# Kernel tuning notes

Measured on AMD Instinct MI355X. Metric: run time of the kernel, lower is better.

Reference implementation:

```python
import jax, jax.numpy as jnp
import numpy as np

N = 32768  # number of leaf states (rows); power of 2 for a clean Fenwick tree
D = 256    # embed_dim


def tree_cell(W, b, hl, cl, hr, cr):
    """Binary TreeLSTM cell: gates from [h_l; h_r], per-child forget gates."""
    z = jnp.concatenate([hl, hr], axis=-1) @ W + b  # [*, 5D]
    i, o, u, fl, fr = jnp.split(z, 5, axis=-1)
    c = jax.nn.sigmoid(i) * jnp.tanh(u) + jax.nn.sigmoid(fl) * cl + jax.nn.sigmoid(fr) * cr
    h = jax.nn.sigmoid(o) * jnp.tanh(c)
    return h, c


def setup_inputs() -> dict:
    key = jax.random.key(0)
    ks = jax.random.split(key, 6)
    s = 0.05  # glorot-ish scale for 512-fan-in weights
    return {
        "h_bot": jax.random.normal(ks[0], (N, D), jnp.float32),
        "c_bot": jax.random.normal(ks[1], (N, D), jnp.float32),
        "W_merge": jax.random.normal(ks[2], (2 * D, 5 * D), jnp.float32) * s,
        "b_merge": jnp.zeros((5 * D,), jnp.float32),
        "W_sum": jax.random.normal(ks[3], (2 * D, 5 * D), jnp.float32) * s,
        "b_sum": jnp.zeros((5 * D,), jnp.float32),
    }


def _fenwick(h_bot, c_bot, W_merge, b_merge, W_sum, b_sum):
    L = N.bit_length() - 1  # 15 tree levels above the leaves
    # --- build Fenwick tree: level k node j covers leaves [j*2^k, (j+1)*2^k) ---
    levels_h, levels_c = [h_bot], [c_bot]
    for k in range(1, L + 1):
        ph, pc = levels_h[-1], levels_c[-1]
        h, c = tree_cell(W_merge, b_merge, ph[0::2], pc[0::2], ph[1::2], pc[1::2])
        levels_h.append(h)
        levels_c.append(c)
    # --- per-prefix summary: for each t in 1..N fold the set-bit nodes of t ---
    # (matches FenwickTree.forward: levels ascending, state = summary(state, node))
    t = jnp.arange(1, N + 1)
    state_h = jnp.zeros((N, D), h_bot.dtype)
    state_c = jnp.zeros((N, D), h_bot.dtype)
    valid = jnp.zeros((N,), bool)
    for k in range(L + 1):
        has = (((t >> k) & 1) == 1)
        # node covering the trailing 2^k block of prefix t at level k
        idx = jnp.clip((t >> (k + 1)) * 2, 0, levels_h[k].shape[0] - 1)
        node_h = levels_h[k][idx]  # irregular gather  [N, D]
        node_c = levels_c[k][idx]
        nh, nc = tree_cell(W_sum, b_sum, state_h, state_c, node_h, node_c)
        m, v = has[:, None], valid[:, None]
        state_h = jnp.where(m, jnp.where(v, nh, node_h), state_h)
        state_c = jnp.where(m, jnp.where(v, nc, node_c), state_c)
        valid = valid | has
    return jnp.concatenate([state_h, state_c], axis=-1)  # [N, 2D]: (row_h, row_c)


def reference(h_bot, c_bot, W_merge, b_merge, W_sum, b_sum):
    return _fenwick(h_bot, c_bot, W_merge, b_merge, W_sum, b_sum)
```

## Files before the change

kernel.cpp:

```cpp
#include <hip/hip_runtime.h>
#include <hip/hip_bf16.h>


typedef unsigned short u16;
typedef unsigned int u32;
using short8  = __attribute__((ext_vector_type(8))) short;
using float4v = __attribute__((ext_vector_type(4))) float;


__device__ __forceinline__ u16 f2bf(float f) {
  u32 u = __float_as_uint(f);
  u = (u + 0x7FFFu + ((u >> 16) & 1u)) >> 16;
  return (u16)u;
}
__device__ __forceinline__ float bf2f(u16 h) {
  return __uint_as_float(((u32)h) << 16);
}
__device__ __forceinline__ float sigf(float x) { return 1.0f / (1.0f + __expf(-x)); }
__device__ __forceinline__ float tanhfast(float x) {
  return 2.0f / (1.0f + __expf(-2.0f * x)) - 1.0f;
}

__device__ __forceinline__ void async16(const void* g, void* l) {
  __builtin_amdgcn_global_load_lds((const __attribute__((address_space(1))) void*)g,
                                   (__attribute__((address_space(3))) void*)l,
                                   16, 0, 0);
}

__device__ __forceinline__ void row_srcs(int mode, int k, int row,
                                         const u16* h0b, const u16* hlv,
                                         const u16* sthA, const u16* sthB,
                                         const u16*& pL, const u16*& pR) {
  if (mode == 0) {
    const u16* pb = (k == 1) ? h0b : (hlv + (size_t)(32768 - (1 << (17 - k))) * 256);
    pL = pb + (size_t)(2 * row) * 256;
    pR = pb + (size_t)(2 * row + 1) * 256;
  } else {
    const int Dk = (1 << k) - 1;
    const int i = row + row / Dk + 1;
    const int t = ((i >> k) << (k + 1)) | (1 << k) | (i & Dk);
    const int c = __popc(i & Dk);
    const u16* sb = (c & 1) ? sthB : sthA;
    pL = sb + (size_t)(t - 1) * 256;
    const int idx = (t >> (k + 1)) * 2;
    pR = hlv + (size_t)((32768 - (1 << (16 - k))) + idx) * 256;
  }
}

__global__ __launch_bounds__(256) void gemm_cell(
    int mode, int k, int Mc,
    const u16* WT, const float* bias,
    const u16* h0b, const u16* hlv, u16* sthA, u16* sthB,
    const float* cpar, float* cout, u16* hout,
    const float* clv, float* out)
{
  __shared__ __align__(16) u16 smem[36864];
  const int tid  = threadIdx.x;
  const int lane = tid & 63;
  const int w    = tid >> 6;
  const int wm   = w >> 1, wn = w & 1;

  const int nwg = gridDim.x;
  const int q8  = nwg >> 3;
  const int id  = (blockIdx.x & 7) * q8 + (blockIdx.x >> 3);
  const int bm  = id >> 3, bn = id & 7;

  const int rr  = lane >> 3;
  const int seg = lane & 7;
  const int swz = ((seg ^ rr) - seg) * 8;

  const u16 *aL[4], *aR[4];
#pragma unroll
  for (int j = 0; j < 4; ++j) {
    int rl = bm * 128 + (w * 4 + j) * 8 + rr;
    if (rl > Mc - 1) rl = Mc - 1;
    const u16 *pL, *pR;
    row_srcs(mode, k, rl, h0b, hlv, sthA, sthB, pL, pR);
    aL[j] = pL + seg * 8 + swz;
    aR[j] = pR + seg * 8 + swz;
  }
  const u16* pB[5];
#pragma unroll
  for (int j = 0; j < 5; ++j)
    pB[j] = WT + (size_t)(bn * 160 + (w * 5 + j) * 8 + rr) * 512 + seg * 8 + swz;

  float4v acc[4][5];
#pragma unroll
  for (int i = 0; i < 4; ++i)
#pragma unroll
    for (int j = 0; j < 5; ++j) acc[i][j] = (float4v){0.f, 0.f, 0.f, 0.f};

  const int mrow = lane & 15;
  const int kg   = lane >> 4;
  const int m7   = mrow & 7;

#define STAGE(buf, kk2)                                                        \
  {                                                                            \
    const int offA = (kk2 & 3) * 64;                                           \
    _Pragma("unroll")                                                          \
    for (int j = 0; j < 4; ++j)                                                \
      async16(((kk2) < 4 ? aL[j] : aR[j]) + offA,                              \
              smem + (buf) * 8192 + (w * 4 + j) * 512);                        \
    _Pragma("unroll")                                                          \
    for (int j = 0; j < 5; ++j)                                                \
      async16(pB[j] + (kk2) * 64,                                              \
              smem + 16384 + (buf) * 10240 + (w * 5 + j) * 512);               \
  }

  STAGE(0, 0);
  __syncthreads();

#pragma unroll
  for (int s = 0; s < 8; ++s) {
    const int cur = s & 1;
    if (s < 7) STAGE(cur ^ 1, s + 1);
    const u16* aT = smem + cur * 8192;
    const u16* bT = smem + 16384 + cur * 10240;
#pragma unroll
    for (int kkk = 0; kkk < 2; ++kkk) {
      short8 af[4], bfv[5];
      const int js = ((kkk * 4 + kg) ^ m7) * 8;
#pragma unroll
      for (int mt = 0; mt < 4; ++mt)
        af[mt] = *(const short8*)(aT + (wm * 64 + mt * 16 + mrow) * 64 + js);
#pragma unroll
      for (int g = 0; g < 5; ++g)
        bfv[g] = *(const short8*)(bT + (g * 32 + wn * 16 + mrow) * 64 + js);
      __builtin_amdgcn_s_setprio(1);
#pragma unroll
      for (int mt = 0; mt < 4; ++mt)
#pragma unroll
        for (int g = 0; g < 5; ++g)
          acc[mt][g] = __builtin_amdgcn_mfma_f32_16x16x32_bf16(af[mt], bfv[g], acc[mt][g], 0, 0, 0);
      __builtin_amdgcn_s_setprio(0);
    }
    __syncthreads();
  }
#undef STAGE

  const int d = bn * 32 + wn * 16 + mrow;
  const float bi  = bias[d];
  const float bo_ = bias[256 + d];
  const float bu  = bias[512 + d];
  const float bfl = bias[768 + d];
  const float bfr2= bias[1024 + d];

#pragma unroll
  for (int mt = 0; mt < 4; ++mt) {
    const int r0 = bm * 128 + wm * 64 + mt * 16 + kg * 4;
#pragma unroll
    for (int r = 0; r < 4; ++r) {
      const int row = r0 + r;
      if (row >= Mc) continue;
      const float zi  = acc[mt][0][r] + bi;
      const float zo  = acc[mt][1][r] + bo_;
      const float zu  = acc[mt][2][r] + bu;
      const float zfl = acc[mt][3][r] + bfl;
      const float zfr = acc[mt][4][r] + bfr2;
      if (mode == 0) {
        const float cl = cpar[(size_t)(2 * row) * 256 + d];
        const float cr = cpar[(size_t)(2 * row + 1) * 256 + d];
        const float c = sigf(zi) * tanhfast(zu) + sigf(zfl) * cl + sigf(zfr) * cr;
        const float h = sigf(zo) * tanhfast(c);
        cout[(size_t)row * 256 + d] = c;
        hout[(size_t)row * 256 + d] = f2bf(h);
      } else {
        const int Dk  = (1 << k) - 1;
        const int i   = row + row / Dk + 1;
        const int t   = ((i >> k) << (k + 1)) | (1 << k) | (i & Dk);
        const int lk  = 32768 - (1 << (16 - k));
        const int idx = (t >> (k + 1)) * 2;
        const float cr = clv[(size_t)(lk + idx) * 256 + d];
        const float cl = out[(size_t)(t - 1) * 512 + 256 + d];
        const float c = sigf(zi) * tanhfast(zu) + sigf(zfl) * cl + sigf(zfr) * cr;
        const float h = sigf(zo) * tanhfast(c);
        out[(size_t)(t - 1) * 512 + 256 + d] = c;
        if ((i >> k) == 0) {
          out[(size_t)(t - 1) * 512 + d] = h;
        } else {
          const int cpc = __popc(i & Dk);
          u16* dst = (cpc & 1) ? sthA : sthB;
          dst[(size_t)(t - 1) * 256 + d] = f2bf(h);
        }
      }
    }
  }
}

__global__ __launch_bounds__(256) void copy_k0(
    const float* __restrict__ h_bot, const float* __restrict__ c_bot,
    float* __restrict__ out, u16* __restrict__ sthB)
{
  const int i = blockIdx.x;
  const int d = threadIdx.x;
  const int t = 2 * i + 1;
  const float h = h_bot[(size_t)(t - 1) * 256 + d];
  const float c = c_bot[(size_t)(t - 1) * 256 + d];
  if (i == 0) out[(size_t)(t - 1) * 512 + d] = h;
  out[(size_t)(t - 1) * 512 + 256 + d] = c;
  sthB[(size_t)(t - 1) * 256 + d] = f2bf(h);
}

__global__ __launch_bounds__(256) void seed_even(
    const u16* __restrict__ hlv, const float* __restrict__ clv,
    float* __restrict__ out, u16* __restrict__ sthB)
{
  const int j = blockIdx.x;
  const int t = 2 * j + 2;
  const int d = threadIdx.x;
  const int k = __ffs(t) - 1;
  const int lk = 32768 - (1 << (16 - k));
  const int nidx = (t >> (k + 1)) * 2;
  const u16 hb  = hlv[(size_t)(lk + nidx) * 256 + d];
  const float c = clv[(size_t)(lk + nidx) * 256 + d];
  out[(size_t)(t - 1) * 512 + 256 + d] = c;
  if ((t & (t - 1)) == 0) {
    out[(size_t)(t - 1) * 512 + d] = bf2f(hb);
  } else {
    sthB[(size_t)(t - 1) * 256 + d] = hb;
  }
}

__global__ __launch_bounds__(256) void transpose_w(
    const float* __restrict__ W, u16* __restrict__ WT)
{
  const int n = blockIdx.x;
  const int b = n / 160, r = n % 160;
  const int g = r / 32,  dl = r % 32;
  const int col = g * 256 + b * 32 + dl;
  const int tid = threadIdx.x;
  WT[(size_t)n * 512 + tid]       = f2bf(W[(size_t)tid * 1280 + col]);
  WT[(size_t)n * 512 + tid + 256] = f2bf(W[(size_t)(tid + 256) * 1280 + col]);
}

__global__ __launch_bounds__(256) void cast_h0(
    const float* __restrict__ h, u16* __restrict__ h0b)
{
  const size_t i = (size_t)blockIdx.x * 256 + threadIdx.x;
  h0b[i] = f2bf(h[i]);
}

extern "C" void kernel_launch(void* const* d_in, const int* in_sizes, int n_in,
                              void* d_out, int out_size, void* d_ws, size_t ws_size,
                              hipStream_t stream) {
  const float* h_bot = (const float*)d_in[0];
  const float* c_bot = (const float*)d_in[1];
  const float* Wm    = (const float*)d_in[2];
  const float* bmv   = (const float*)d_in[3];
  const float* Wsu   = (const float*)d_in[4];
  const float* bsv   = (const float*)d_in[5];
  float* out = (float*)d_out;
  char* ws = (char*)d_ws;

  u16*   WmT  = (u16*)(ws + 0);
  u16*   WsT  = (u16*)(ws + 1310720);
  u16*   h0b  = (u16*)(ws + 2621440);
  u16*   hlv  = (u16*)(ws + 19398656);
  float* clv  = (float*)(ws + 36175872);
  u16*   sthA = (u16*)(ws + 69730304);
  u16*   sthB = (u16*)(ws + 86507520);

  transpose_w<<<1280, 256, 0, stream>>>(Wm, WmT);
  transpose_w<<<1280, 256, 0, stream>>>(Wsu, WsT);
  cast_h0<<<32768, 256, 0, stream>>>(h_bot, h0b);

  for (int kl = 1; kl <= 15; ++kl) {
    const int M = 32768 >> kl;
    const float* cpar = (kl == 1) ? c_bot : (clv + (size_t)(32768 - (1 << (17 - kl))) * 256);
    float* cout = clv + (size_t)(32768 - (1 << (16 - kl))) * 256;
    u16*   hout = hlv + (size_t)(32768 - (1 << (16 - kl))) * 256;
    const int nbm = (M + 127) / 128;
    gemm_cell<<<nbm * 8, 256, 0, stream>>>(0, kl, M, WmT, bmv, h0b, hlv,
                                           sthA, sthB,
                                           cpar, cout, hout, clv, out);
  }

  copy_k0<<<16384, 256, 0, stream>>>(h_bot, c_bot, out, sthB);
  seed_even<<<16384, 256, 0, stream>>>(hlv, clv, out, sthB);
  for (int kl = 1; kl <= 14; ++kl) {
    const int M = 16384 - (16384 >> kl);
    const int nbm = (M + 127) / 128;
    gemm_cell<<<nbm * 8, 256, 0, stream>>>(1, kl, M, WsT, bsv, h0b, hlv,
                                           sthA, sthB,
                                           nullptr, nullptr, nullptr, clv, out);
  }
}
```

Baseline: 984.2 us.

## Deepen GEMM LDS pipeline to four stages with finer K-steps and manual waitcnts

Reworks the GEMM main loop from a two-buffer, 64-wide K-step pipeline into a four-buffer, 32-wide K-step pipeline with three stages prefetched ahead. It uses explicit vmcnt waits and raw s_barrier instead of __syncthreads, so global-to-LDS loads overlap more with MFMA work. The LDS tile layout, swizzle and per-thread load assignment change to match. The risks are a hand-counted vmcnt schedule that must match the per-wave issue counts, and more loop iterations with barriers.

```diff
diff --git a/kernel.cpp b/kernel.cpp
--- a/kernel.cpp
+++ b/kernel.cpp
@@ -65,24 +65,23 @@
   const int id  = (blockIdx.x & 7) * q8 + (blockIdx.x >> 3);
   const int bm  = id >> 3, bn = id & 7;
 
-  const int rr  = lane >> 3;
-  const int seg = lane & 7;
-  const int swz = ((seg ^ rr) - seg) * 8;
-
-  const u16 *aL[4], *aR[4];
-#pragma unroll
-  for (int j = 0; j < 4; ++j) {
-    int rl = bm * 128 + (w * 4 + j) * 8 + rr;
-    if (rl > Mc - 1) rl = Mc - 1;
-    const u16 *pL, *pR;
-    row_srcs(mode, k, rl, h0b, hlv, sthA, sthB, pL, pR);
-    aL[j] = pL + seg * 8 + swz;
-    aR[j] = pR + seg * 8 + swz;
-  }
-  const u16* pB[5];
-#pragma unroll
-  for (int j = 0; j < 5; ++j)
-    pB[j] = WT + (size_t)(bn * 160 + (w * 5 + j) * 8 + rr) * 512 + seg * 8 + swz;
+  const int f0 = w * 128 + lane;
+  const int f1 = f0 + 64;
+  int rl0 = bm * 128 + (f0 >> 2); if (rl0 > Mc - 1) rl0 = Mc - 1;
+  int rl1 = bm * 128 + (f1 >> 2); if (rl1 > Mc - 1) rl1 = Mc - 1;
+  const u16 *p0L, *p0R, *p1L, *p1R;
+  row_srcs(mode, k, rl0, h0b, hlv, sthA, sthB, p0L, p0R);
+  row_srcs(mode, k, rl1, h0b, hlv, sthA, sthB, p1L, p1R);
+  const int sa0 = ((f0 & 3) ^ ((f0 >> 3) & 3)) * 8;
+  const int sa1 = ((f1 & 3) ^ ((f1 >> 3) & 3)) * 8;
+
+  const int ch0 = w, ch1 = 4 + w, ch2 = 8 + w;
+  const int sb = ((lane & 3) ^ ((lane >> 3) & 3)) * 8;
+  const u16* pB0 = WT + (size_t)(bn * 160 + ch0 * 16 + (lane >> 2)) * 512 + sb;
+  const u16* pB1 = WT + (size_t)(bn * 160 + ch1 * 16 + (lane >> 2)) * 512 + sb;
+  const u16* pB2 = (w < 2)
+      ? WT + (size_t)(bn * 160 + ch2 * 16 + (lane >> 2)) * 512 + sb
+      : pB0;
 
   float4v acc[4][5];
 #pragma unroll
@@ -92,49 +91,59 @@
 
   const int mrow = lane & 15;
   const int kg   = lane >> 4;
-  const int m7   = mrow & 7;
-
-#define STAGE(buf, kk2)                                                        \
-  {                                                                            \
-    const int offA = (kk2 & 3) * 64;                                           \
-    _Pragma("unroll")                                                          \
-    for (int j = 0; j < 4; ++j)                                                \
-      async16(((kk2) < 4 ? aL[j] : aR[j]) + offA,                              \
-              smem + (buf) * 8192 + (w * 4 + j) * 512);                        \
-    _Pragma("unroll")                                                          \
-    for (int j = 0; j < 5; ++j)                                                \
-      async16(pB[j] + (kk2) * 64,                                              \
-              smem + 16384 + (buf) * 10240 + (w * 5 + j) * 512);               \
-  }
-
-  STAGE(0, 0);
-  __syncthreads();
-
-#pragma unroll
-  for (int s = 0; s < 8; ++s) {
-    const int cur = s & 1;
-    if (s < 7) STAGE(cur ^ 1, s + 1);
-    const u16* aT = smem + cur * 8192;
-    const u16* bT = smem + 16384 + cur * 10240;
-#pragma unroll
-    for (int kkk = 0; kkk < 2; ++kkk) {
-      short8 af[4], bfv[5];
-      const int js = ((kkk * 4 + kg) ^ m7) * 8;
-#pragma unroll
-      for (int mt = 0; mt < 4; ++mt)
-        af[mt] = *(const short8*)(aT + (wm * 64 + mt * 16 + mrow) * 64 + js);
+  const int ks   = (kg ^ ((mrow >> 1) & 3)) * 8;
+  const u16* aBase = smem + (wm * 64 + mrow) * 32 + ks;
+  const u16* bBase = smem + 4096 + (wn * 16 + mrow) * 32 + ks;
+
+#define STAGE(buf, kk)                                                          \
+  {                                                                             \
+    const int co = ((kk) & 7) * 32;                                             \
+    async16((((kk) < 8) ? p0L : p0R) + sa0 + co,                                \
+            smem + (buf) * 9216 + (w * 2 + 0) * 512);                           \
+    async16((((kk) < 8) ? p1L : p1R) + sa1 + co,                                \
+            smem + (buf) * 9216 + (w * 2 + 1) * 512);                           \
+    async16(pB0 + (kk) * 32, smem + (buf) * 9216 + 4096 + ch0 * 512);           \
+    async16(pB1 + (kk) * 32, smem + (buf) * 9216 + 4096 + ch1 * 512);           \
+    if (w < 2)                                                                  \
+      async16(pB2 + (kk) * 32, smem + (buf) * 9216 + 4096 + ch2 * 512);         \
+  }
+
+  STAGE(0, 0); STAGE(1, 1); STAGE(2, 2);
+  if (w < 2) { asm volatile("s_waitcnt vmcnt(10)" ::: "memory"); }
+  else       { asm volatile("s_waitcnt vmcnt(8)"  ::: "memory"); }
+  __builtin_amdgcn_s_barrier();
+
+#pragma unroll
+  for (int s = 0; s < 16; ++s) {
+    const int cur = s & 3;
+    if (s + 3 < 16) STAGE((s + 3) & 3, s + 3);
+    short8 af[4], bfv[5];
+    const u16* aB = aBase + cur * 9216;
+    const u16* bB = bBase + cur * 9216;
+#pragma unroll
+    for (int mt = 0; mt < 4; ++mt) af[mt] = *(const short8*)(aB + mt * 512);
+#pragma unroll
+    for (int g = 0; g < 5; ++g)   bfv[g] = *(const short8*)(bB + g * 1024);
+    asm volatile("s_waitcnt lgkmcnt(0)" ::: "memory");
+    __builtin_amdgcn_sched_barrier(0);
+    __builtin_amdgcn_s_setprio(1);
+#pragma unroll
+    for (int mt = 0; mt < 4; ++mt)
 #pragma unroll
       for (int g = 0; g < 5; ++g)
-        bfv[g] = *(const short8*)(bT + (g * 32 + wn * 16 + mrow) * 64 + js);
-      __builtin_amdgcn_s_setprio(1);
-#pragma unroll
-      for (int mt = 0; mt < 4; ++mt)
-#pragma unroll
-        for (int g = 0; g < 5; ++g)
-          acc[mt][g] = __builtin_amdgcn_mfma_f32_16x16x32_bf16(af[mt], bfv[g], acc[mt][g], 0, 0, 0);
-      __builtin_amdgcn_s_setprio(0);
+        acc[mt][g] = __builtin_amdgcn_mfma_f32_16x16x32_bf16(af[mt], bfv[g], acc[mt][g], 0, 0, 0);
+    __builtin_amdgcn_s_setprio(0);
+    __builtin_amdgcn_sched_barrier(0);
+    if (s < 13) {
+      if (w < 2) { asm volatile("s_waitcnt vmcnt(10)" ::: "memory"); }
+      else       { asm volatile("s_waitcnt vmcnt(8)"  ::: "memory"); }
+    } else if (s == 13) {
+      if (w < 2) { asm volatile("s_waitcnt vmcnt(5)" ::: "memory"); }
+      else       { asm volatile("s_waitcnt vmcnt(4)" ::: "memory"); }
+    } else if (s == 14) {
+      asm volatile("s_waitcnt vmcnt(0)" ::: "memory");
     }
-    __syncthreads();
+    if (s < 15) __builtin_amdgcn_s_barrier();
   }
 #undef STAGE
 
```

Result: slower. 1.030 ms (+4.6%).

## Load GEMM fragments directly from global memory, dropping LDS staging

Applied to the files above, without the earlier changes.

Removes the double-buffered global_load_lds staging through shared memory and the per-stage barriers. Each wave now loads its MFMA A and B fragments straight from global memory as 16-byte vectors, over two K loops (left child, then right child). A launch bound of 3 blocks per CU is added to raise occupancy now that no LDS is used. The cost is that rows are no longer shared between waves through LDS, so each fragment is re-read from global/L2 by several waves, and loads are exposed without explicit prefetch overlap.

```diff
diff --git a/kernel.cpp b/kernel.cpp
--- a/kernel.cpp
+++ b/kernel.cpp
@@ -19,12 +19,6 @@
 __device__ __forceinline__ float sigf(float x) { return 1.0f / (1.0f + __expf(-x)); }
 __device__ __forceinline__ float tanhfast(float x) {
   return 2.0f / (1.0f + __expf(-2.0f * x)) - 1.0f;
-}
-
-__device__ __forceinline__ void async16(const void* g, void* l) {
-  __builtin_amdgcn_global_load_lds((const __attribute__((address_space(1))) void*)g,
-                                   (__attribute__((address_space(3))) void*)l,
-                                   16, 0, 0);
 }
 
 __device__ __forceinline__ void row_srcs(int mode, int k, int row,
@@ -47,14 +41,13 @@
   }
 }
 
-__global__ __launch_bounds__(256) void gemm_cell(
+__global__ __launch_bounds__(256, 3) void gemm_cell(
     int mode, int k, int Mc,
     const u16* WT, const float* bias,
     const u16* h0b, const u16* hlv, u16* sthA, u16* sthB,
     const float* cpar, float* cout, u16* hout,
     const float* clv, float* out)
 {
-  __shared__ __align__(16) u16 smem[36864];
   const int tid  = threadIdx.x;
   const int lane = tid & 63;
   const int w    = tid >> 6;
@@ -65,24 +58,23 @@
   const int id  = (blockIdx.x & 7) * q8 + (blockIdx.x >> 3);
   const int bm  = id >> 3, bn = id & 7;
 
-  const int rr  = lane >> 3;
-  const int seg = lane & 7;
-  const int swz = ((seg ^ rr) - seg) * 8;
-
-  const u16 *aL[4], *aR[4];
-#pragma unroll
-  for (int j = 0; j < 4; ++j) {
-    int rl = bm * 128 + (w * 4 + j) * 8 + rr;
+  const int mrow = lane & 15;
+  const int kg   = lane >> 4;
+
+  const u16 *rL[4], *rR[4];
+#pragma unroll
+  for (int mt = 0; mt < 4; ++mt) {
+    int rl = bm * 128 + wm * 64 + mt * 16 + mrow;
     if (rl > Mc - 1) rl = Mc - 1;
     const u16 *pL, *pR;
     row_srcs(mode, k, rl, h0b, hlv, sthA, sthB, pL, pR);
-    aL[j] = pL + seg * 8 + swz;
-    aR[j] = pR + seg * 8 + swz;
-  }
-  const u16* pB[5];
-#pragma unroll
-  for (int j = 0; j < 5; ++j)
-    pB[j] = WT + (size_t)(bn * 160 + (w * 5 + j) * 8 + rr) * 512 + seg * 8 + swz;
+    rL[mt] = pL + kg * 8;
+    rR[mt] = pR + kg * 8;
+  }
+  const u16* bp[5];
+#pragma unroll
+  for (int g = 0; g < 5; ++g)
+    bp[g] = WT + (size_t)(bn * 160 + g * 32 + wn * 16 + mrow) * 512 + kg * 8;
 
   float4v acc[4][5];
 #pragma unroll
@@ -90,53 +82,36 @@
 #pragma unroll
     for (int j = 0; j < 5; ++j) acc[i][j] = (float4v){0.f, 0.f, 0.f, 0.f};
 
-  const int mrow = lane & 15;
-  const int kg   = lane >> 4;
-  const int m7   = mrow & 7;
-
-#define STAGE(buf, kk2)                                                        \
-  {                                                                            \
-    const int offA = (kk2 & 3) * 64;                                           \
-    _Pragma("unroll")                                                          \
-    for (int j = 0; j < 4; ++j)                                                \
-      async16(((kk2) < 4 ? aL[j] : aR[j]) + offA,                              \
-              smem + (buf) * 8192 + (w * 4 + j) * 512);                        \
-    _Pragma("unroll")                                                          \
-    for (int j = 0; j < 5; ++j)                                                \
-      async16(pB[j] + (kk2) * 64,                                              \
-              smem + 16384 + (buf) * 10240 + (w * 5 + j) * 512);               \
-  }
-
-  STAGE(0, 0);
-  __syncthreads();
-
-#pragma unroll
-  for (int s = 0; s < 8; ++s) {
-    const int cur = s & 1;
-    if (s < 7) STAGE(cur ^ 1, s + 1);
-    const u16* aT = smem + cur * 8192;
-    const u16* bT = smem + 16384 + cur * 10240;
-#pragma unroll
-    for (int kkk = 0; kkk < 2; ++kkk) {
-      short8 af[4], bfv[5];
-      const int js = ((kkk * 4 + kg) ^ m7) * 8;
-#pragma unroll
-      for (int mt = 0; mt < 4; ++mt)
-        af[mt] = *(const short8*)(aT + (wm * 64 + mt * 16 + mrow) * 64 + js);
+#pragma unroll
+  for (int kk = 0; kk < 8; ++kk) {
+    short8 af[4], bfv[5];
+#pragma unroll
+    for (int mt = 0; mt < 4; ++mt) af[mt] = *(const short8*)(rL[mt] + kk * 32);
+#pragma unroll
+    for (int g = 0; g < 5; ++g)   bfv[g] = *(const short8*)(bp[g] + kk * 32);
+    __builtin_amdgcn_s_setprio(1);
+#pragma unroll
+    for (int mt = 0; mt < 4; ++mt)
 #pragma unroll
       for (int g = 0; g < 5; ++g)
-        bfv[g] = *(const short8*)(bT + (g * 32 + wn * 16 + mrow) * 64 + js);
-      __builtin_amdgcn_s_setprio(1);
-#pragma unroll
-      for (int mt = 0; mt < 4; ++mt)
-#pragma unroll
-        for (int g = 0; g < 5; ++g)
-          acc[mt][g] = __builtin_amdgcn_mfma_f32_16x16x32_bf16(af[mt], bfv[g], acc[mt][g], 0, 0, 0);
-      __builtin_amdgcn_s_setprio(0);
-    }
-    __syncthreads();
-  }
-#undef STAGE
+        acc[mt][g] = __builtin_amdgcn_mfma_f32_16x16x32_bf16(af[mt], bfv[g], acc[mt][g], 0, 0, 0);
+    __builtin_amdgcn_s_setprio(0);
+  }
+#pragma unroll
+  for (int kk = 0; kk < 8; ++kk) {
+    short8 af[4], bfv[5];
+#pragma unroll
+    for (int mt = 0; mt < 4; ++mt) af[mt] = *(const short8*)(rR[mt] + kk * 32);
+#pragma unroll
+    for (int g = 0; g < 5; ++g)   bfv[g] = *(const short8*)(bp[g] + 256 + kk * 32);
+    __builtin_amdgcn_s_setprio(1);
+#pragma unroll
+    for (int mt = 0; mt < 4; ++mt)
+#pragma unroll
+      for (int g = 0; g < 5; ++g)
+        acc[mt][g] = __builtin_amdgcn_mfma_f32_16x16x32_bf16(af[mt], bfv[g], acc[mt][g], 0, 0, 0);
+    __builtin_amdgcn_s_setprio(0);
+  }
 
   const int d = bn * 32 + wn * 16 + mrow;
   const float bi  = bias[d];
```

Result: slower. 1.596 ms (+62.1%).
